# Performance work log

Measured on AMD Instinct MI355X. Metric: run time of the kernel, lower is better.

The kernel has to match this reference:

```python
import jax, jax.numpy as jnp
import numpy as np

STRIDE = 1
KSIZE = 3
DEMOD = True


def _conv_single(xi, wi, pad):
    # xi: [C,H,W], wi: [O,C,k,k] -> [O,H,W]
    out = jax.lax.conv_general_dilated(
        xi[None], wi, window_strides=(STRIDE, STRIDE),
        padding=[(pad, pad), (pad, pad)],
        dimension_numbers=("NCHW", "OIHW", "NCHW"))
    return out[0]


def setup_inputs() -> dict:
    key = jax.random.key(0)
    ks = jax.random.split(key, 6)
    B, Cin, Cout, S, H, W = 8, 512, 512, 512, 64, 64
    return {
        "x": jax.random.normal(ks[0], (B, Cin, H, W), jnp.float32),
        "y": jax.random.normal(ks[1], (B, S), jnp.float32),
        "affine_w": jax.random.normal(ks[2], (Cin, S), jnp.float32) * 0.02,
        "affine_b": jax.random.normal(ks[3], (Cin,), jnp.float32) * 0.02,
        "weight": jax.random.normal(ks[4], (Cout, Cin, KSIZE, KSIZE), jnp.float32) * 0.05,
        "bias": jax.random.normal(ks[5], (1, Cout, 1, 1), jnp.float32) * 0.02,
    }


def reference(x, y, affine_w, affine_b, weight, bias):
    B, _, H, W = x.shape
    style_dim = affine_w.shape[1]
    coef = 1.0 / np.sqrt(style_dim)  # ELR: gain / sqrt(fan_in)
    # style modulation scale per input channel: [B, Cin]
    s = (y * coef) @ affine_w.T + affine_b + 1.0
    # per-sample weights: [B, O, I, k, k]
    w = weight[None, :, :, :, :] * s[:, None, :, None, None]
    if DEMOD:
        d = jax.lax.rsqrt(jnp.sum(w * w, axis=(2, 3, 4), keepdims=True) + 1e-4)
        w = w * d
    pad = ((H - 1) * (STRIDE - 1) + (KSIZE - 1)) // 2
    out = jax.vmap(lambda xi, wi: _conv_single(xi, wi, pad))(x, w)  # [B,O,H,W]
    return out + bias
```

## Files before the change

kernel.cpp:

```cpp
#include <hip/hip_runtime.h>

typedef __attribute__((ext_vector_type(8))) short short8;
typedef __attribute__((ext_vector_type(4))) float floatx4;
typedef unsigned short u16;
typedef unsigned int u32;

#define NB 8
#define CI 512
#define CO 512
#define HH 64
#define WW 64
#define HP 66
#define WP 66
#define BK 64

__device__ __forceinline__ u16 f2bf(float f) {
  u32 u = __builtin_bit_cast(u32, f);
  u += 0x7fffu + ((u >> 16) & 1u);
  return (u16)(u >> 16);
}

__device__ __forceinline__ void gload16(const void* g, void* l) {
  __builtin_amdgcn_global_load_lds(
      (const __attribute__((address_space(1))) unsigned int*)g,
      (__attribute__((address_space(3))) unsigned int*)l, 16, 0, 0);
}

__global__ __launch_bounds__(256) void k_prep1(
    const float* __restrict__ y, const float* __restrict__ aw,
    const float* __restrict__ ab, float* __restrict__ s,
    const float* __restrict__ wt, float* __restrict__ wsum,
    u16* __restrict__ wbv)
{
  if (blockIdx.x < 1024) {
    const int wid = blockIdx.x * 4 + (threadIdx.x >> 6);
    const int lane = threadIdx.x & 63;
    const int b = wid >> 9, i = wid & 511;
    float sum = 0.f;
    #pragma unroll
    for (int j = 0; j < 8; ++j) {
      const int k = lane + (j << 6);
      sum += y[b * CI + k] * aw[i * CI + k];
    }
    #pragma unroll
    for (int off = 32; off; off >>= 1) sum += __shfl_xor(sum, off);
    if (lane == 0) s[wid] = sum * 0.044194173824159216f + ab[i] + 1.0f;
  } else {
    const int idx = (blockIdx.x - 1024) * 256 + threadIdx.x;
    const int i = idx & 511;
    const int o = idx >> 9;
    const float* p = wt + (size_t)idx * 9;
    float v[9];
    float sum = 0.f;
    #pragma unroll
    for (int t = 0; t < 9; ++t) { v[t] = p[t]; sum += v[t] * v[t]; }
    wsum[idx] = sum;
    #pragma unroll
    for (int t = 0; t < 9; ++t) wbv[(((o * 9 + t) << 9) | i)] = f2bf(v[t]);
  }
}

__global__ __launch_bounds__(256) void k_xfd(
    const float* __restrict__ x, const float* __restrict__ s,
    u16* __restrict__ xs, const float* __restrict__ wsum,
    float* __restrict__ d)
{
  __shared__ __align__(16) u16 lds[64 * 72];
  if (blockIdx.x >= 4096) {
    const int wid = (blockIdx.x - 4096) * 4 + (threadIdx.x >> 6);
    const int lane = threadIdx.x & 63;
    const int b = wid >> 9, o = wid & 511;
    float sum = 0.f;
    #pragma unroll
    for (int j = 0; j < 8; ++j) {
      const int i = lane + (j << 6);
      const float sv = s[b * CI + i];
      sum += wsum[o * CI + i] * sv * sv;
    }
    #pragma unroll
    for (int off = 32; off; off >>= 1) sum += __shfl_xor(sum, off);
    if (lane == 0) d[wid] = rsqrtf(sum + 1e-4f);
    return;
  }
  const int blk = blockIdx.x;
  const int ic = blk & 7;
  const int h = (blk >> 3) & 63;
  const int b = blk >> 9;
  const int i0 = ic << 6;
  const int t = threadIdx.x;
  const int w = t & 63;
  const int i4 = t >> 6;
  #pragma unroll
  for (int p = 0; p < 16; ++p) {
    const int ii = i4 + (p << 2);
    const float xv = x[((size_t)(b * CI + i0 + ii) * HH + h) * WW + w];
    const float sv = s[b * CI + i0 + ii];
    lds[w * 72 + ii] = f2bf(xv * sv);
  }
  const uint4 z4 = {0u, 0u, 0u, 0u};
  if (t < 16) {
    const int wside = (t < 8) ? 0 : 65;
    const int q = t & 7;
    *(uint4*)&xs[((size_t)(b * HP + h + 1) * WP + wside) * CI + i0 + (q << 3)] = z4;
  }
  if (h == 0) {
    for (int idx = t; idx < 2 * 66 * 8; idx += 256) {
      const int row = (idx < 528) ? 0 : 65;
      const int rem = (idx < 528) ? idx : idx - 528;
      const int wz = rem >> 3;
      const int q = rem & 7;
      *(uint4*)&xs[((size_t)(b * HP + row) * WP + wz) * CI + i0 + (q << 3)] = z4;
    }
  }
  __syncthreads();
  const int w2 = t >> 2;
  const int q = t & 3;
  const uint4* src = (const uint4*)&lds[w2 * 72 + (q << 4)];
  const uint4 v0 = src[0];
  const uint4 v1 = src[1];
  u16* dst = xs + ((size_t)(b * HP + h + 1) * WP + (w2 + 1)) * CI + i0 + (q << 4);
  *(uint4*)dst = v0;
  *((uint4*)dst + 1) = v1;
}

__global__ __launch_bounds__(512, 2) void k_conv(
    const u16* __restrict__ xs, const u16* __restrict__ wb,
    const float* __restrict__ dmod, const float* __restrict__ bias,
    float* __restrict__ out)
{
  __shared__ __align__(16) u16 lA[2 * 16384];
  __shared__ __align__(16) u16 lB[2 * 16384];

  const int blk = blockIdx.x;
  const int nt = blk & 15;
  const int mt = (blk >> 4) & 1;
  const int b  = blk >> 5;
  const int ob = mt << 8;
  const int p0 = nt << 8;

  const int tid = threadIdx.x;
  const int wid = tid >> 6;
  const int lane = tid & 63;
  const int col = lane & 15;
  const int k8  = lane >> 4;
  const int wr  = wid >> 2;
  const int wc  = wid & 3;

  const int lr = lane >> 3;
  const int ls = lane & 7;
  const int swz = ls ^ lr;

  u32 aoff[4], boff[4], ldst[4];
  #pragma unroll
  for (int h2 = 0; h2 < 4; ++h2) {
    const int rowBase = ((h2 >> 1) << 7) + (wid << 4) + ((h2 & 1) << 3);
    const int rowIdx = rowBase + lr;
    aoff[h2] = (u32)((ob + rowIdx) * 4608 + (swz << 3));
    const int p = p0 + rowIdx;
    boff[h2] = (u32)(((b * HP + (p >> 6)) * WP + (p & 63)) * 512 + (swz << 3));
    ldst[h2] = (u32)(rowBase << 6);
  }

  const u32 sA0 = (u32)(((0 + k8) ^ (col & 7)) << 3);
  const u32 sA1 = (u32)(((4 + k8) ^ (col & 7)) << 3);
  const u32 aRead = (u32)((((wr << 7) + col) << 6));
  const u32 bRead = (u32)((((wc << 6) + col) << 6));

  floatx4 acc[8][4];
  #pragma unroll
  for (int m = 0; m < 8; ++m)
    #pragma unroll
    for (int n = 0; n < 4; ++n)
      acc[m][n] = (floatx4){0.f, 0.f, 0.f, 0.f};

  short8 a0[4][2], b0[2][2], b1[2][2];

#define SA(TILE, H, BUF) do {                                                 \
    const u32 at_ = (u32)((TILE) << 6);                                       \
    gload16(wb + aoff[(H)*2+0] + at_, &lA[((BUF) << 14) + ldst[(H)*2+0]]);    \
    gload16(wb + aoff[(H)*2+1] + at_, &lA[((BUF) << 14) + ldst[(H)*2+1]]);    \
  } while (0)

#define SB(TILE, H, BUF) do {                                                 \
    const int t_ = (TILE);                                                    \
    const int tap_ = t_ >> 3;                                                 \
    const int kh_ = tap_ / 3;                                                 \
    const int kw_ = tap_ - kh_ * 3;                                           \
    const u32 bt_ = (u32)(((kh_ * WP + kw_) << 9) + ((t_ & 7) << 6));         \
    gload16(xs + boff[(H)*2+0] + bt_, &lB[((BUF) << 14) + ldst[(H)*2+0]]);    \
    gload16(xs + boff[(H)*2+1] + bt_, &lB[((BUF) << 14) + ldst[(H)*2+1]]);    \
  } while (0)

#define READ_A(PA, MH) do {                                                   \
    _Pragma("unroll")                                                         \
    for (int mq = 0; mq < 4; ++mq) {                                          \
      a0[mq][0] = *(const short8*)((PA) + (MH) * 4096 + mq * 1024 + sA0);     \
      a0[mq][1] = *(const short8*)((PA) + (MH) * 4096 + mq * 1024 + sA1);     \
    }                                                                         \
  } while (0)

#define READ_B(PB, NH, BV) do {                                               \
    _Pragma("unroll")                                                         \
    for (int nq = 0; nq < 2; ++nq) {                                          \
      BV[nq][0] = *(const short8*)((PB) + (NH) * 2048 + nq * 1024 + sA0);     \
      BV[nq][1] = *(const short8*)((PB) + (NH) * 2048 + nq * 1024 + sA1);     \
    }                                                                         \
  } while (0)

#define MFMA_Q(MH, NH, BV) do {                                               \
    _Pragma("unroll")                                                         \
    for (int kk = 0; kk < 2; ++kk)                                            \
      _Pragma("unroll")                                                       \
      for (int nq = 0; nq < 2; ++nq)                                          \
        _Pragma("unroll")                                                     \
        for (int mq = 0; mq < 4; ++mq)                                        \
          acc[(MH)*4+mq][(NH)*2+nq] = __builtin_amdgcn_mfma_f32_16x16x32_bf16(\
              a0[mq][kk], BV[nq][kk], acc[(MH)*4+mq][(NH)*2+nq], 0, 0, 0);    \
  } while (0)

#define SBAR __builtin_amdgcn_s_barrier()
#define SCH0 __builtin_amdgcn_sched_barrier(0)
#define PRI1 __builtin_amdgcn_s_setprio(1)
#define PRI0 __builtin_amdgcn_s_setprio(0)

#define TILE4(T, C, MODE) do {                                                \
    const u16* pA  = lA + ((C) << 14) + aRead;                                \
    const u16* pB  = lB + ((C) << 14) + bRead;                                \
    const u16* pBn = lB + ((1 - (C)) << 14) + bRead;                          \
         \
    READ_A(pA, 0);                                                            \
    SCH0; if (MODE >= 1) SA((T) + 1, 0, 1 - (C));                             \
    SBAR; PRI1; MFMA_Q(0, 0, b0); PRI0; SBAR;                                 \
                                     \
    READ_B(pB, 1, b1);                                                        \
    SCH0; if (MODE >= 1) SA((T) + 1, 1, 1 - (C));                             \
    SBAR; PRI1; MFMA_Q(0, 1, b1); PRI0; SBAR;                                 \
             \
    READ_A(pA, 1);                                                            \
    SCH0; if (MODE == 2) SB((T) + 2, 0, C);                                   \
    if (MODE == 2)      asm volatile("s_waitcnt vmcnt(6)" ::: "memory");      \
    else if (MODE == 1) asm volatile("s_waitcnt vmcnt(4)" ::: "memory");      \
    SBAR; PRI1; MFMA_Q(1, 1, b1); PRI0; SBAR;                                 \
                  \
    SCH0; if (MODE == 2) SB((T) + 2, 1, C);                                   \
    if (MODE == 2)      asm volatile("s_waitcnt vmcnt(4)" ::: "memory");      \
    else if (MODE == 1) asm volatile("s_waitcnt vmcnt(0)" ::: "memory");      \
    SBAR; PRI1; MFMA_Q(1, 0, b0); PRI0;                                       \
    if (MODE >= 1) READ_B(pBn, 0, b0);                                        \
    SBAR;                                                                     \
  } while (0)

  SB(0, 0, 0); SB(0, 1, 0);
  SA(0, 0, 0); SA(0, 1, 0);
  SB(1, 0, 1); SB(1, 1, 1);
  asm volatile("s_waitcnt vmcnt(4)" ::: "memory");
  SCH0;
  SBAR;
  {
    const u16* pB0 = lB + bRead;
    READ_B(pB0, 0, b0);
  }

  for (int j = 0; j < 35; ++j) {
    TILE4(2 * j,     0, 2);
    TILE4(2 * j + 1, 1, 2);
  }
  TILE4(70, 0, 1);
  TILE4(71, 1, 0);

#undef SA
#undef SB
#undef READ_A
#undef READ_B
#undef MFMA_Q
#undef TILE4
#undef SBAR
#undef SCH0
#undef PRI1
#undef PRI0

  #pragma unroll
  for (int m = 0; m < 8; ++m) {
    #pragma unroll
    for (int r = 0; r < 4; ++r) {
      const int o = ob + (wr << 7) + (m << 4) + (k8 << 2) + r;
      const float dm = dmod[b * CO + o];
      const float bs = bias[o];
      float* po = out + (((size_t)(b * CO + o)) << 12) + p0 + (wc << 6);
      #pragma unroll
      for (int n = 0; n < 4; ++n)
        po[(n << 4) + col] = acc[m][n][r] * dm + bs;
    }
  }
}

extern "C" void kernel_launch(void* const* d_in, const int* in_sizes, int n_in,
                              void* d_out, int out_size, void* d_ws, size_t ws_size,
                              hipStream_t stream) {
  const float* x    = (const float*)d_in[0];
  const float* y    = (const float*)d_in[1];
  const float* aw   = (const float*)d_in[2];
  const float* ab   = (const float*)d_in[3];
  const float* wt   = (const float*)d_in[4];
  const float* bias = (const float*)d_in[5];
  float* out = (float*)d_out;

  char* ws = (char*)d_ws;
  const size_t XS_BYTES = (size_t)NB * HP * WP * CI * 2;
  const size_t WB_BYTES = (size_t)CO * 9 * CI * 2;
  const size_t WS_BYTES = (size_t)CO * CI * 4;
  u16* xsb    = (u16*)ws;
  u16* wbuf   = (u16*)(ws + XS_BYTES);
  float* wsum = (float*)(ws + XS_BYTES + WB_BYTES);
  float* sbuf = (float*)(ws + XS_BYTES + WB_BYTES + WS_BYTES);
  float* dbuf = sbuf + NB * CI;

  k_prep1<<<dim3(2048), dim3(256), 0, stream>>>(y, aw, ab, sbuf, wt, wsum, wbuf);
  k_xfd  <<<dim3(5120), dim3(256), 0, stream>>>(x, sbuf, xsb, wsum, dbuf);
  k_conv <<<dim3(256), dim3(512), 0, stream>>>(xsb, wbuf, dbuf, bias, out);
}
```

Baseline: 154.2 us.

## Use 4 waves per block with 128x128 warp tiles and reordered MFMA schedule

The conv GEMM block shrinks from 8 waves to 4 waves, each computing a 128x128 output tile (8x8 accumulators) instead of 128x64. This raises register-level reuse of A and B fragments and halves the LDS reads per MFMA. The LDS prefetch schedule is reordered around a two-set A register double buffer with explicit lgkmcnt waits. In exchange, register pressure rises sharply (256 accumulator floats per lane) and there are fewer waves per CU to hide latency.

```diff
diff --git a/kernel.cpp b/kernel.cpp
--- a/kernel.cpp
+++ b/kernel.cpp
@@ -123,7 +123,7 @@
   *((uint4*)dst + 1) = v1;
 }
 
-__global__ __launch_bounds__(512, 2) void k_conv(
+__global__ __launch_bounds__(256, 1) void k_conv(
     const u16* __restrict__ xs, const u16* __restrict__ wb,
     const float* __restrict__ dmod, const float* __restrict__ bias,
     float* __restrict__ out)
@@ -143,42 +143,43 @@
   const int lane = tid & 63;
   const int col = lane & 15;
   const int k8  = lane >> 4;
-  const int wr  = wid >> 2;
-  const int wc  = wid & 3;
+  const int wr  = wid >> 1;
+  const int wc  = wid & 1;
 
   const int lr = lane >> 3;
   const int ls = lane & 7;
   const int swz = ls ^ lr;
 
-  u32 aoff[4], boff[4], ldst[4];
+  u32 aoff[8], boff[8], ldst[8];
   #pragma unroll
-  for (int h2 = 0; h2 < 4; ++h2) {
-    const int rowBase = ((h2 >> 1) << 7) + (wid << 4) + ((h2 & 1) << 3);
+  for (int i = 0; i < 8; ++i) {
+    const int rowBase = ((i >> 2) << 7) + (wid << 5) + ((i & 3) << 3);
     const int rowIdx = rowBase + lr;
-    aoff[h2] = (u32)((ob + rowIdx) * 4608 + (swz << 3));
+    aoff[i] = (u32)((ob + rowIdx) * 4608 + (swz << 3));
     const int p = p0 + rowIdx;
-    boff[h2] = (u32)(((b * HP + (p >> 6)) * WP + (p & 63)) * 512 + (swz << 3));
-    ldst[h2] = (u32)(rowBase << 6);
+    boff[i] = (u32)(((b * HP + (p >> 6)) * WP + (p & 63)) * 512 + (swz << 3));
+    ldst[i] = (u32)(rowBase << 6);
   }
 
   const u32 sA0 = (u32)(((0 + k8) ^ (col & 7)) << 3);
   const u32 sA1 = (u32)(((4 + k8) ^ (col & 7)) << 3);
   const u32 aRead = (u32)((((wr << 7) + col) << 6));
-  const u32 bRead = (u32)((((wc << 6) + col) << 6));
-
-  floatx4 acc[8][4];
+  const u32 bRead = (u32)((((wc << 7) + col) << 6));
+
+  floatx4 acc[8][8];
   #pragma unroll
   for (int m = 0; m < 8; ++m)
     #pragma unroll
-    for (int n = 0; n < 4; ++n)
+    for (int n = 0; n < 8; ++n)
       acc[m][n] = (floatx4){0.f, 0.f, 0.f, 0.f};
 
-  short8 a0[4][2], b0[2][2], b1[2][2];
+  short8 a0[4][2], a1[4][2], b0[4][2], b1[4][2];
 
 #define SA(TILE, H, BUF) do {                                                 \
     const u32 at_ = (u32)((TILE) << 6);                                       \
-    gload16(wb + aoff[(H)*2+0] + at_, &lA[((BUF) << 14) + ldst[(H)*2+0]]);    \
-    gload16(wb + aoff[(H)*2+1] + at_, &lA[((BUF) << 14) + ldst[(H)*2+1]]);    \
+    _Pragma("unroll")                                                         \
+    for (int g = 0; g < 4; ++g)                                               \
+      gload16(wb + aoff[(H)*4+g] + at_, &lA[((BUF) << 14) + ldst[(H)*4+g]]);  \
   } while (0)
 
 #define SB(TILE, H, BUF) do {                                                 \
@@ -187,35 +188,36 @@
     const int kh_ = tap_ / 3;                                                 \
     const int kw_ = tap_ - kh_ * 3;                                           \
     const u32 bt_ = (u32)(((kh_ * WP + kw_) << 9) + ((t_ & 7) << 6));         \
-    gload16(xs + boff[(H)*2+0] + bt_, &lB[((BUF) << 14) + ldst[(H)*2+0]]);    \
-    gload16(xs + boff[(H)*2+1] + bt_, &lB[((BUF) << 14) + ldst[(H)*2+1]]);    \
-  } while (0)
-
-#define READ_A(PA, MH) do {                                                   \
+    _Pragma("unroll")                                                         \
+    for (int g = 0; g < 4; ++g)                                               \
+      gload16(xs + boff[(H)*4+g] + bt_, &lB[((BUF) << 14) + ldst[(H)*4+g]]);  \
+  } while (0)
+
+#define READ_AH(SET, PA, MH) do {                                             \
     _Pragma("unroll")                                                         \
     for (int mq = 0; mq < 4; ++mq) {                                          \
-      a0[mq][0] = *(const short8*)((PA) + (MH) * 4096 + mq * 1024 + sA0);     \
-      a0[mq][1] = *(const short8*)((PA) + (MH) * 4096 + mq * 1024 + sA1);     \
+      SET[mq][0] = *(const short8*)((PA) + ((MH)*4+mq) * 1024 + sA0);         \
+      SET[mq][1] = *(const short8*)((PA) + ((MH)*4+mq) * 1024 + sA1);         \
     }                                                                         \
   } while (0)
 
-#define READ_B(PB, NH, BV) do {                                               \
-    _Pragma("unroll")                                                         \
-    for (int nq = 0; nq < 2; ++nq) {                                          \
-      BV[nq][0] = *(const short8*)((PB) + (NH) * 2048 + nq * 1024 + sA0);     \
-      BV[nq][1] = *(const short8*)((PB) + (NH) * 2048 + nq * 1024 + sA1);     \
+#define READ_BH(BV, PB, NH) do {                                              \
+    _Pragma("unroll")                                                         \
+    for (int nq = 0; nq < 4; ++nq) {                                          \
+      BV[nq][0] = *(const short8*)((PB) + ((NH)*4+nq) * 1024 + sA0);          \
+      BV[nq][1] = *(const short8*)((PB) + ((NH)*4+nq) * 1024 + sA1);          \
     }                                                                         \
   } while (0)
 
-#define MFMA_Q(MH, NH, BV) do {                                               \
+#define MFMA_Q(MH, NH, ASET, BV) do {                                         \
     _Pragma("unroll")                                                         \
     for (int kk = 0; kk < 2; ++kk)                                            \
       _Pragma("unroll")                                                       \
-      for (int nq = 0; nq < 2; ++nq)                                          \
+      for (int nq = 0; nq < 4; ++nq)                                          \
         _Pragma("unroll")                                                     \
         for (int mq = 0; mq < 4; ++mq)                                        \
-          acc[(MH)*4+mq][(NH)*2+nq] = __builtin_amdgcn_mfma_f32_16x16x32_bf16(\
-              a0[mq][kk], BV[nq][kk], acc[(MH)*4+mq][(NH)*2+nq], 0, 0, 0);    \
+          acc[(MH)*4+mq][(NH)*4+nq] = __builtin_amdgcn_mfma_f32_16x16x32_bf16(\
+              ASET[mq][kk], BV[nq][kk], acc[(MH)*4+mq][(NH)*4+nq], 0, 0, 0);  \
   } while (0)
 
 #define SBAR __builtin_amdgcn_s_barrier()
@@ -226,39 +228,50 @@
 #define TILE4(T, C, MODE) do {                                                \
     const u16* pA  = lA + ((C) << 14) + aRead;                                \
     const u16* pB  = lB + ((C) << 14) + bRead;                                \
+    const u16* pAn = lA + ((1 - (C)) << 14) + aRead;                          \
     const u16* pBn = lB + ((1 - (C)) << 14) + bRead;                          \
-         \
-    READ_A(pA, 0);                                                            \
-    SCH0; if (MODE >= 1) SA((T) + 1, 0, 1 - (C));                             \
-    SBAR; PRI1; MFMA_Q(0, 0, b0); PRI0; SBAR;                                 \
-                                     \
-    READ_B(pB, 1, b1);                                                        \
+                  \
+    if (MODE >= 1) SA((T) + 1, 0, 1 - (C));                                   \
+    SBAR;                                                                     \
+    asm volatile("s_waitcnt lgkmcnt(8)" ::: "memory"); SCH0;                  \
+    PRI1; MFMA_Q(0, 0, a0, b0); PRI0;                                         \
+    READ_AH(a1, pA, 1);                                                       \
+                                   \
     SCH0; if (MODE >= 1) SA((T) + 1, 1, 1 - (C));                             \
-    SBAR; PRI1; MFMA_Q(0, 1, b1); PRI0; SBAR;                                 \
-             \
-    READ_A(pA, 1);                                                            \
+    SBAR;                                                                     \
+    asm volatile("s_waitcnt lgkmcnt(0)" ::: "memory"); SCH0;                  \
+    PRI1; MFMA_Q(1, 0, a1, b0); PRI0;                                         \
+                                    \
     SCH0; if (MODE == 2) SB((T) + 2, 0, C);                                   \
-    if (MODE == 2)      asm volatile("s_waitcnt vmcnt(6)" ::: "memory");      \
-    else if (MODE == 1) asm volatile("s_waitcnt vmcnt(4)" ::: "memory");      \
-    SBAR; PRI1; MFMA_Q(1, 1, b1); PRI0; SBAR;                                 \
+    SBAR;                                                                     \
+    if (MODE == 2)      asm volatile("s_waitcnt vmcnt(12)" ::: "memory");     \
+    else if (MODE == 1) asm volatile("s_waitcnt vmcnt(8)" ::: "memory");      \
+    SCH0;                                                                     \
+    if (MODE >= 1) READ_BH(b0, pBn, 0);                                       \
+    SCH0;                                                                     \
+    PRI1; MFMA_Q(1, 1, a1, b1); PRI0;                                         \
                   \
     SCH0; if (MODE == 2) SB((T) + 2, 1, C);                                   \
-    if (MODE == 2)      asm volatile("s_waitcnt vmcnt(4)" ::: "memory");      \
+    SBAR;                                                                     \
+    if (MODE == 2)      asm volatile("s_waitcnt vmcnt(8)" ::: "memory");      \
     else if (MODE == 1) asm volatile("s_waitcnt vmcnt(0)" ::: "memory");      \
-    SBAR; PRI1; MFMA_Q(1, 0, b0); PRI0;                                       \
-    if (MODE >= 1) READ_B(pBn, 0, b0);                                        \
-    SBAR;                                                                     \
+    SCH0;                                                                     \
+    PRI1; MFMA_Q(0, 1, a0, b1); PRI0;                                         \
+    if (MODE >= 1) { READ_AH(a0, pAn, 0); READ_BH(b1, pBn, 1); }              \
   } while (0)
 
   SB(0, 0, 0); SB(0, 1, 0);
   SA(0, 0, 0); SA(0, 1, 0);
   SB(1, 0, 1); SB(1, 1, 1);
-  asm volatile("s_waitcnt vmcnt(4)" ::: "memory");
+  asm volatile("s_waitcnt vmcnt(8)" ::: "memory");
   SCH0;
   SBAR;
   {
+    const u16* pA0 = lA + aRead;
     const u16* pB0 = lB + bRead;
-    READ_B(pB0, 0, b0);
+    READ_AH(a0, pA0, 0);
+    READ_BH(b0, pB0, 0);
+    READ_BH(b1, pB0, 1);
   }
 
   for (int j = 0; j < 35; ++j) {
@@ -270,8 +283,8 @@
 
 #undef SA
 #undef SB
-#undef READ_A
-#undef READ_B
+#undef READ_AH
+#undef READ_BH
 #undef MFMA_Q
 #undef TILE4
 #undef SBAR
@@ -286,9 +299,9 @@
       const int o = ob + (wr << 7) + (m << 4) + (k8 << 2) + r;
       const float dm = dmod[b * CO + o];
       const float bs = bias[o];
-      float* po = out + (((size_t)(b * CO + o)) << 12) + p0 + (wc << 6);
+      float* po = out + (((size_t)(b * CO + o)) << 12) + p0 + (wc << 7);
       #pragma unroll
-      for (int n = 0; n < 4; ++n)
+      for (int n = 0; n < 8; ++n)
         po[(n << 4) + col] = acc[m][n][r] * dm + bs;
     }
   }
@@ -317,5 +330,5 @@
 
   k_prep1<<<dim3(2048), dim3(256), 0, stream>>>(y, aw, ab, sbuf, wt, wsum, wbuf);
   k_xfd  <<<dim3(5120), dim3(256), 0, stream>>>(x, sbuf, xsb, wsum, dbuf);
-  k_conv <<<dim3(256), dim3(512), 0, stream>>>(xsb, wbuf, dbuf, bias, out);
-}
+  k_conv <<<dim3(256), dim3(256), 0, stream>>>(xsb, wbuf, dbuf, bias, out);
+}
```

Result: slower. 256.7 us (+66.4%).
